# Performance work log

Measured on AMD Instinct MI355X. Metric: run time of the kernel, lower is better.

The kernel has to match this reference:

```python
import jax, jax.numpy as jnp
import numpy as np

N = 20000
E = 100000
IN_CH = 512
OUT_CH = 256
HID = 2 * OUT_CH          # 512
CAT = 5 * HID             # 2560
BN_EPS = 1e-5


def _sage(x, src, dst, w_edge, Wl, Wr, b):
    """PyG SAGEConv (mean aggr): lin_l(mean_{j->i} x_j) + lin_r(x_i).
    w_edge: per-edge float weight (0/1 mask); messages flow src -> dst."""
    msg = x[src] * w_edge[:, None]                              # [E, F]
    s = jax.ops.segment_sum(msg, dst, num_segments=N)           # [N, F]
    cnt = jax.ops.segment_sum(w_edge, dst, num_segments=N)      # [N]
    mean = s / jnp.maximum(cnt, 1.0)[:, None]
    return mean @ Wl.T + x @ Wr.T + b


def setup_inputs() -> dict:
    key = jax.random.key(0)
    ks = jax.random.split(key, 12)
    x = jax.random.normal(ks[0], (N, IN_CH), dtype=jnp.float32)
    edge_index = jax.random.randint(ks[1], (2, E), 0, N, dtype=jnp.int64)
    edge_attr = jax.random.randint(ks[2], (E,), 0, 5, dtype=jnp.int64)
    sc = 1.0 / np.sqrt(IN_CH)
    Wl5 = jax.random.uniform(ks[3], (5, HID, IN_CH), jnp.float32, -sc, sc)
    Wr5 = jax.random.uniform(ks[4], (5, HID, IN_CH), jnp.float32, -sc, sc)
    bl5 = jnp.zeros((5, HID), jnp.float32)
    sc2 = 1.0 / np.sqrt(CAT)
    Wmu_l = jax.random.uniform(ks[5], (OUT_CH, CAT), jnp.float32, -sc2, sc2)
    Wmu_r = jax.random.uniform(ks[6], (OUT_CH, CAT), jnp.float32, -sc2, sc2)
    bmu = jnp.zeros((OUT_CH,), jnp.float32)
    Wlv_l = jax.random.uniform(ks[7], (OUT_CH, CAT), jnp.float32, -sc2, sc2)
    Wlv_r = jax.random.uniform(ks[8], (OUT_CH, CAT), jnp.float32, -sc2, sc2)
    blv = jnp.zeros((OUT_CH,), jnp.float32)
    gamma = jnp.ones((CAT,), jnp.float32)
    beta = jnp.zeros((CAT,), jnp.float32)
    run_mean = jax.random.normal(ks[9], (CAT,), jnp.float32) * 0.1
    run_var = jnp.abs(jax.random.normal(ks[10], (CAT,), jnp.float32)) + 1.0
    return {"x": x, "edge_index": edge_index, "edge_attr": edge_attr,
            "Wl5": Wl5, "Wr5": Wr5, "bl5": bl5,
            "Wmu_l": Wmu_l, "Wmu_r": Wmu_r, "bmu": bmu,
            "Wlv_l": Wlv_l, "Wlv_r": Wlv_r, "blv": blv,
            "gamma": gamma, "beta": beta,
            "run_mean": run_mean, "run_var": run_var}


def reference(x, edge_index, edge_attr, Wl5, Wr5, bl5,
              Wmu_l, Wmu_r, bmu, Wlv_l, Wlv_r, blv,
              gamma, beta, run_mean, run_var):
    # eval mode: all dropouts are identity, BatchNorm uses running stats.
    src, dst = edge_index[0], edge_index[1]
    # 5 relation branches: mask edges by relation id instead of nonzero slicing
    branches = []
    for k in range(5):
        w = (edge_attr == k).astype(x.dtype)                    # [E]
        h = _sage(x, src, dst, w, Wl5[k], Wr5[k], bl5[k])       # [N, HID]
        branches.append(jax.nn.relu(h))
    h = jnp.concatenate(branches, axis=1)                       # [N, CAT]
    # BatchNorm1d (eval)
    h = (h - run_mean) * jax.lax.rsqrt(run_var + BN_EPS) * gamma + beta
    ones = jnp.ones((E,), x.dtype)
    mu = _sage(h, src, dst, ones, Wmu_l, Wmu_r, bmu)            # [N, OUT_CH]
    logvar = _sage(h, src, dst, ones, Wlv_l, Wlv_r, blv)        # [N, OUT_CH]
    return (mu, logvar)
```

## Files before the change

### kernel.cpp

```cpp
#include <hip/hip_runtime.h>
#include <stdint.h>

#define INCH 512
#define HIDW 512
#define CATW 2560
#define OUTW 256
#define BN_EPS 1e-5f
#define TS 1024

typedef __bf16 bf16x8 __attribute__((ext_vector_type(8)));
typedef float f32x4 __attribute__((ext_vector_type(4)));

__device__ __forceinline__ unsigned short f2bf(float f) {
  union { float f; unsigned u; } v; v.f = f;
  unsigned r = v.u + 0x7FFFu + ((v.u >> 16) & 1u);
  return (unsigned short)(r >> 16);
}

__device__ __forceinline__ float bf2f(unsigned short u) {
  union { unsigned u; float f; } v; v.u = ((unsigned)u) << 16; return v.f;
}

__device__ __forceinline__ void pack4(unsigned short* dst, float a, float b, float c, float d) {
  unsigned lo = (unsigned)f2bf(a) | ((unsigned)f2bf(b) << 16);
  unsigned hi = (unsigned)f2bf(c) | ((unsigned)f2bf(d) << 16);
  *reinterpret_cast<uint2*>(dst) = make_uint2(lo, hi);
}


__global__ void cvt_bf16_kernel(const float* __restrict__ in, unsigned short* __restrict__ out, int n4) {
  int g = blockIdx.x * blockDim.x + threadIdx.x;
  if (g >= n4) return;
  int base = g * 4;
  float4 v = *reinterpret_cast<const float4*>(in + base);
  pack4(out + base, v.x, v.y, v.z, v.w);
}

__global__ void pack_w1p_kernel(const float* __restrict__ Wl, const float* __restrict__ Wr,
                                unsigned short* __restrict__ out) {
  int g = blockIdx.x * blockDim.x + threadIdx.x;
  if (g >= 5 * 128 * 512) return;
  int z = g >> 16;
  int rem = g & 65535;
  int c = rem >> 9;
  int j = rem & 511;
  int kk = c * 8;
  const float* src = (kk < 512) ? (Wl + ((size_t)(z * 512 + j)) * 512 + kk)
                                : (Wr + ((size_t)(z * 512 + j)) * 512 + (kk - 512));
  float4 a = *reinterpret_cast<const float4*>(src);
  float4 b = *reinterpret_cast<const float4*>(src + 4);
  pack4(out + (size_t)g * 8, a.x, a.y, a.z, a.w);
  pack4(out + (size_t)g * 8 + 4, b.x, b.y, b.z, b.w);
}

__global__ void pack_w23p_kernel(const float* __restrict__ Wmu_l, const float* __restrict__ Wlv_l,
                                 const float* __restrict__ Wmu_r, const float* __restrict__ Wlv_r,
                                 unsigned short* __restrict__ out) {
  int g = blockIdx.x * blockDim.x + threadIdx.x;
  if (g >= 320 * 1024) return;
  int c = g >> 10;
  int j = g & 1023;
  const float* row;
  if (j < 256)       row = Wmu_l + (size_t)j * CATW;
  else if (j < 512)  row = Wlv_l + (size_t)(j - 256) * CATW;
  else if (j < 768)  row = Wmu_r + (size_t)(j - 512) * CATW;
  else               row = Wlv_r + (size_t)(j - 768) * CATW;
  const float* src = row + c * 8;
  float4 a = *reinterpret_cast<const float4*>(src);
  float4 b = *reinterpret_cast<const float4*>(src + 4);
  pack4(out + (size_t)g * 8, a.x, a.y, a.z, a.w);
  pack4(out + (size_t)g * 8 + 4, b.x, b.y, b.z, b.w);
}


__global__ void hist_kernel(const int* __restrict__ ei, const int* __restrict__ ea,
                            int* __restrict__ cnt, int E) {
  int e = blockIdx.x * 256 + threadIdx.x;
  if (e >= E) return;
  atomicAdd(&cnt[ei[E + e] * 5 + ea[e]], 1);
}

__global__ void scan1_kernel(const int* __restrict__ in, int* __restrict__ out,
                             int* __restrict__ bsum, int n) {
  __shared__ int lds[256];
  int t = threadIdx.x;
  int base = blockIdx.x * TS + t * 4;
  int4 v = make_int4(0, 0, 0, 0);
  if (base + 3 < n) v = *reinterpret_cast<const int4*>(in + base);
  else {
    if (base < n) v.x = in[base];
    if (base + 1 < n) v.y = in[base + 1];
    if (base + 2 < n) v.z = in[base + 2];
    if (base + 3 < n) v.w = in[base + 3];
  }
  int s = v.x + v.y + v.z + v.w;
  lds[t] = s;
  __syncthreads();
  for (int o = 1; o < 256; o <<= 1) {
    int a = (t >= o) ? lds[t - o] : 0;
    __syncthreads();
    lds[t] += a;
    __syncthreads();
  }
  int excl = lds[t] - s;
  if (t == 255) bsum[blockIdx.x] = lds[255];
  int e0 = excl, e1 = e0 + v.x, e2 = e1 + v.y, e3 = e2 + v.z;
  if (base < n) out[base] = e0;
  if (base + 1 < n) out[base + 1] = e1;
  if (base + 2 < n) out[base + 2] = e2;
  if (base + 3 < n) out[base + 3] = e3;
}

__global__ void scan2_kernel(int* __restrict__ bsum, int nb) {
  __shared__ int lds[128];
  int t = threadIdx.x;
  int v = (t < nb) ? bsum[t] : 0;
  lds[t] = v;
  __syncthreads();
  for (int o = 1; o < 128; o <<= 1) {
    int a = (t >= o) ? lds[t - o] : 0;
    __syncthreads();
    lds[t] += a;
    __syncthreads();
  }
  if (t < nb) bsum[t] = lds[t] - v;
}

__global__ void scan3_kernel(int* __restrict__ out, const int* __restrict__ bsum,
                             int n, int total) {
  int g = blockIdx.x * 256 + threadIdx.x;
  if (g == 0) out[n] = total;
  int base = g * 4;
  if (base >= n) return;
  int add = bsum[base / TS];
  if (base + 3 < n) {
    int4 v = *reinterpret_cast<int4*>(out + base);
    v.x += add; v.y += add; v.z += add; v.w += add;
    *reinterpret_cast<int4*>(out + base) = v;
  } else {
    for (int q = 0; q < 4 && base + q < n; ++q) out[base + q] += add;
  }
}

__global__ void fill_kernel(const int* __restrict__ ei, const int* __restrict__ ea,
                            const int* __restrict__ offs, int* __restrict__ fillc,
                            int* __restrict__ perm, int E) {
  int e = blockIdx.x * 256 + threadIdx.x;
  if (e >= E) return;
  int key = ei[E + e] * 5 + ea[e];
  int p = atomicAdd(&fillc[key], 1);
  perm[offs[key] + p] = ei[e];
}


__global__ void gather1_kernel(const unsigned short* __restrict__ xb, const int* __restrict__ offs,
                               const int* __restrict__ perm, unsigned short* __restrict__ meanb5) {
  int i = blockIdx.x;
  int k = blockIdx.y;
  int t = threadIdx.x;
  int b0 = offs[i * 5 + k], b1 = offs[i * 5 + k + 1];
  float a0 = 0.f, a1 = 0.f, a2 = 0.f, a3 = 0.f;
  for (int e = b0; e < b1; ++e) {
    int s = perm[e];
    ushort4 v = reinterpret_cast<const ushort4*>(xb + (size_t)s * 512)[t];
    a0 += bf2f(v.x); a1 += bf2f(v.y); a2 += bf2f(v.z); a3 += bf2f(v.w);
  }
  float inv = (b1 > b0) ? 1.0f / (float)(b1 - b0) : 0.0f;
  pack4(meanb5 + (size_t)i * CATW + k * 512 + t * 4, a0 * inv, a1 * inv, a2 * inv, a3 * inv);
}

__global__ void gather2_kernel(const float* __restrict__ z, const int* __restrict__ offs,
                               const int* __restrict__ perm, float* __restrict__ dout,
                               const float* __restrict__ bmu, const float* __restrict__ blv,
                               int M) {
  int i = blockIdx.x;
  int t = threadIdx.x;
  int b0 = offs[i * 5], b1 = offs[i * 5 + 5];
  float4 acc = make_float4(0.f, 0.f, 0.f, 0.f);
  for (int e = b0; e < b1; ++e) {
    int s = perm[e];
    float4 v = reinterpret_cast<const float4*>(z + (size_t)s * 512)[t];
    acc.x += v.x; acc.y += v.y; acc.z += v.z; acc.w += v.w;
  }
  float inv = (b1 > b0) ? 1.0f / (float)(b1 - b0) : 1.0f;
  int c = t * 4;
  float* op;
  const float* bp;
  if (c < 256) { op = dout + (size_t)i * OUTW + c; bp = bmu + c; }
  else         { op = dout + (size_t)M * OUTW + (size_t)i * OUTW + (c - 256); bp = blv + (c - 256); }
  float4 y = *reinterpret_cast<float4*>(op);
  float4 b = *reinterpret_cast<const float4*>(bp);
  y.x += acc.x * inv + b.x; y.y += acc.y * inv + b.y;
  y.z += acc.z * inv + b.z; y.w += acc.w * inv + b.w;
  *reinterpret_cast<float4*>(op) = y;
}

template<int MODE>
__global__ __launch_bounds__(256, 3)
void gemm_kernel(const unsigned short* __restrict__ A,
                 const unsigned short* __restrict__ A2,
                 const unsigned short* __restrict__ B,
                 unsigned short* __restrict__ hOut,
                 float* __restrict__ fOut,
                 float* __restrict__ fOut2,
                 const float* __restrict__ p0,
                 const float* __restrict__ p1,
                 const float* __restrict__ p2,
                 const float* __restrict__ p3,
                 const float* __restrict__ p4,
                 int M)
{
  constexpr int KTOT = (MODE == 0) ? (2 * INCH) : CATW;
  constexpr int KT = KTOT / 32;
  constexpr int NBLK = (MODE == 0) ? 4 : 8;
  constexpr int NC = (MODE == 0) ? 512 : 1024;

  const int nwg = gridDim.x;
  const int o = blockIdx.x;
  const int q = nwg >> 3, r = nwg & 7;
  const int xcd = o & 7;
  const int wg = (xcd < r ? xcd * (q + 1) : r * (q + 1) + (xcd - r) * q) + (o >> 3);
  const int rowBase = (wg / NBLK) * 128;
  const int nBase = (wg % NBLK) * 128;
  const int z = (MODE == 0) ? blockIdx.z : 0;
  const unsigned short* BpF = (MODE == 0) ? (B + (size_t)z * 524288) : B;

  __shared__ unsigned short As[4][4096];

  const int tid = threadIdx.x;
  const int lane = tid & 63;
  const int wv = tid >> 6;
  const int wr = wv >> 1, wc = wv & 1;
  const int lr = lane & 15, kg = lane >> 4;

  const int srow0 = (wv * 2) * 16 + (lane >> 2);
  const int srow1 = srow0 + 16;
  const int kswz = (((lane & 3) ^ ((lane >> 4) & 3)) * 8);
  int gar0 = rowBase + srow0; if (gar0 >= M) gar0 = M - 1;
  int gar1 = rowBase + srow1; if (gar1 >= M) gar1 = M - 1;

  int aslot[4];
#pragma unroll
  for (int m = 0; m < 4; ++m) {
    const int ar = wr * 64 + m * 16 + lr;
    aslot[m] = ar * 32 + ((kg ^ ((lr >> 2) & 3)) * 8);
  }

  size_t bjoff[4];
#pragma unroll
  for (int n = 0; n < 4; ++n)
    bjoff[n] = (size_t)(nBase + wc * 64 + n * 16 + lr) * 8;

  f32x4 acc[4][4] = {};

  auto stageA = [&](int slot, int kt) {
    const int kk0 = kt * 32;
    const unsigned short *a0p, *a1p;
    if (MODE == 0) {
      if (kk0 < INCH) {
        a0p = A + (size_t)gar0 * CATW + z * 512 + kk0 + kswz;
        a1p = A + (size_t)gar1 * CATW + z * 512 + kk0 + kswz;
      } else {
        a0p = A2 + (size_t)gar0 * INCH + (kk0 - INCH) + kswz;
        a1p = A2 + (size_t)gar1 * INCH + (kk0 - INCH) + kswz;
      }
    } else {
      a0p = A + (size_t)gar0 * KTOT + kk0 + kswz;
      a1p = A + (size_t)gar1 * KTOT + kk0 + kswz;
    }
    __builtin_amdgcn_global_load_lds((const void*)a0p, (void*)&As[slot][(wv * 2) * 512], 16, 0, 0);
    __builtin_amdgcn_global_load_lds((const void*)a1p, (void*)&As[slot][(wv * 2 + 1) * 512], 16, 0, 0);
  };

  auto loadB = [&](int kt, bf16x8 (&dst)[4]) {
    const size_t cbase = (size_t)((kt << 2) + kg) * NC * 8;
#pragma unroll
    for (int n = 0; n < 4; ++n)
      dst[n] = *reinterpret_cast<const bf16x8*>(BpF + cbase + bjoff[n]);
  };

  auto step = [&](int t, const bf16x8 (&bcur)[4], bf16x8 (&bnxt)[4]) {
    const int slot = t & 3;
    bf16x8 af[4];
#pragma unroll
    for (int m = 0; m < 4; ++m)
      af[m] = *reinterpret_cast<const bf16x8*>(&As[slot][aslot[m]]);
    if (t + 1 < KT) loadB(t + 1, bnxt);
    if (t + 3 < KT) stageA((t + 3) & 3, t + 3);
    __builtin_amdgcn_sched_barrier(0);
    __builtin_amdgcn_s_setprio(1);
#pragma unroll
    for (int m = 0; m < 4; ++m)
#pragma unroll
      for (int n = 0; n < 4; ++n)
        acc[m][n] = __builtin_amdgcn_mfma_f32_16x16x32_bf16(af[m], bcur[n], acc[m][n], 0, 0, 0);
    __builtin_amdgcn_s_setprio(0);
    __builtin_amdgcn_sched_barrier(0);
    __builtin_amdgcn_s_barrier();
    __builtin_amdgcn_sched_barrier(0);
  };

  bf16x8 bP[4], bQ[4];
  stageA(0, 0);
  stageA(1, 1);
  stageA(2, 2);
  __builtin_amdgcn_sched_barrier(0);
  loadB(0, bP);
  __builtin_amdgcn_sched_barrier(0);
  asm volatile("s_waitcnt vmcnt(8)" ::: "memory");
  __builtin_amdgcn_s_barrier();
  __builtin_amdgcn_sched_barrier(0);

  for (int t = 0; t < KT; t += 2) {
    step(t, bP, bQ);
    step(t + 1, bQ, bP);
  }

  if (MODE == 0) {
    unsigned short* lds16 = &As[0][0];
#pragma unroll
    for (int n = 0; n < 4; ++n) {
      const int j = wc * 64 + n * 16 + lr;
      const int ch = z * 512 + nBase + j;
      const float bias = p0[ch];
      const float scale = rsqrtf(p2[ch] + BN_EPS) * p3[ch];
      const float rm = p1[ch], be = p4[ch];
#pragma unroll
      for (int m = 0; m < 4; ++m)
#pragma unroll
        for (int rr = 0; rr < 4; ++rr) {
          const int row = wr * 64 + m * 16 + kg * 4 + rr;
          float v = acc[m][n][rr] + bias;
          v = fmaxf(v, 0.0f);
          v = (v - rm) * scale + be;
          lds16[row * 128 + (j ^ ((row & 7) << 3))] = f2bf(v);
        }
    }
    __syncthreads();
    const int trow = tid >> 4;
    const int cb = tid & 15;
#pragma unroll
    for (int p = 0; p < 8; ++p) {
      const int row = p * 16 + trow;
      const int i = rowBase + row;
      if (i < M) {
        const int scb = cb ^ (row & 7);
        uint4 v = *reinterpret_cast<const uint4*>(&lds16[row * 128 + scb * 8]);
        *reinterpret_cast<uint4*>(&hOut[(size_t)i * CATW + z * 512 + nBase + cb * 8]) = v;
      }
    }
  } else {
    float* ldsf = reinterpret_cast<float*>(&As[0][0]);
#pragma unroll
    for (int hp = 0; hp < 2; ++hp) {
      __syncthreads();
      if (wc == hp) {
#pragma unroll
        for (int n = 0; n < 4; ++n) {
          const int jl = n * 16 + lr;
#pragma unroll
          for (int m = 0; m < 4; ++m)
#pragma unroll
            for (int rr = 0; rr < 4; ++rr) {
              const int row = wr * 64 + m * 16 + kg * 4 + rr;
              ldsf[row * 64 + jl] = acc[m][n][rr];
            }
        }
      }
      __syncthreads();
      const int trow = tid >> 4, cb = tid & 15;
      const int jbase = nBase + hp * 64;
#pragma unroll
      for (int p = 0; p < 8; ++p) {
        const int row = p * 16 + trow;
        const int i = rowBase + row;
        if (i < M) {
          float4 v = *reinterpret_cast<const float4*>(&ldsf[row * 64 + cb * 4]);
          const int j = jbase + cb * 4;
          float* dst;
          if (j < 512) {
            dst = fOut + (size_t)i * 512 + j;
          } else {
            const int jj = j - 512;
            dst = (jj < OUTW) ? (fOut2 + (size_t)i * OUTW + jj)
                              : (fOut2 + (size_t)M * OUTW + (size_t)i * OUTW + (jj - OUTW));
          }
          *reinterpret_cast<float4*>(dst) = v;
        }
      }
    }
  }
}


extern "C" void kernel_launch(void* const* d_in, const int* in_sizes, int n_in,
                              void* d_out, int out_size, void* d_ws, size_t ws_size,
                              hipStream_t stream) {
  const float* x     = (const float*)d_in[0];
  const int*   ei    = (const int*)d_in[1];
  const int*   ea    = (const int*)d_in[2];
  const float* Wl5   = (const float*)d_in[3];
  const float* Wr5   = (const float*)d_in[4];
  const float* bl5   = (const float*)d_in[5];
  const float* Wmu_l = (const float*)d_in[6];
  const float* Wmu_r = (const float*)d_in[7];
  const float* bmu   = (const float*)d_in[8];
  const float* Wlv_l = (const float*)d_in[9];
  const float* Wlv_r = (const float*)d_in[10];
  const float* blv   = (const float*)d_in[11];
  const float* gamma = (const float*)d_in[12];
  const float* beta  = (const float*)d_in[13];
  const float* rmean = (const float*)d_in[14];
  const float* rvar  = (const float*)d_in[15];
  (void)n_in; (void)out_size;

  const int N = in_sizes[0] / INCH;
  const int E = in_sizes[2];
  const int NKEY = N * 5;

  char* ws = (char*)d_ws;
  size_t off = 0;
  auto take = [&](size_t bytes) { char* p = ws + off; off += (bytes + 255) & ~(size_t)255; return p; };
  unsigned short* hb = (unsigned short*)take((size_t)N * CATW * 2);
  char* U = take((size_t)N * CATW * 2);
  unsigned short* xb = (unsigned short*)take((size_t)N * 512 * 2);
  unsigned short* w1p  = (unsigned short*)take((size_t)5 * 128 * 512 * 8 * 2);
  unsigned short* w23p = (unsigned short*)take((size_t)320 * 1024 * 8 * 2);
  int* cntk  = (int*)take((size_t)NKEY * 4);
  int* offs  = (int*)take((size_t)(NKEY + 1) * 4);
  int* fillc = (int*)take((size_t)NKEY * 4);
  int* perm  = (int*)take((size_t)E * 4);
  int* bsum  = (int*)take(256 * 4);
  if (off > ws_size) return;

  unsigned short* meanb5 = (unsigned short*)U;
  float* zbuf  = (float*)U;

  cvt_bf16_kernel<<<dim3((N * INCH / 4 + 255) / 256), 256, 0, stream>>>(x, xb, N * INCH / 4);
  pack_w1p_kernel<<<dim3((5 * 128 * 512 + 255) / 256), 256, 0, stream>>>(Wl5, Wr5, w1p);
  pack_w23p_kernel<<<dim3((320 * 1024 + 255) / 256), 256, 0, stream>>>(Wmu_l, Wlv_l, Wmu_r, Wlv_r, w23p);

  hipMemsetAsync(cntk, 0, (size_t)NKEY * 4, stream);
  hipMemsetAsync(fillc, 0, (size_t)NKEY * 4, stream);
  hist_kernel<<<dim3((E + 255) / 256), 256, 0, stream>>>(ei, ea, cntk, E);
  const int nb = (NKEY + TS - 1) / TS;
  scan1_kernel<<<dim3(nb), 256, 0, stream>>>(cntk, offs, bsum, NKEY);
  scan2_kernel<<<dim3(1), 128, 0, stream>>>(bsum, nb);
  scan3_kernel<<<dim3((NKEY / 4 + 255) / 256 + 1), 256, 0, stream>>>(offs, bsum, NKEY, E);
  fill_kernel<<<dim3((E + 255) / 256), 256, 0, stream>>>(ei, ea, offs, fillc, perm, E);

  gather1_kernel<<<dim3(N, 5), 128, 0, stream>>>(xb, offs, perm, meanb5);
  const int mblk = (N + 127) / 128;
  gemm_kernel<0><<<dim3(mblk * 4, 1, 5), 256, 0, stream>>>(
      meanb5, xb, w1p, hb, nullptr, nullptr,
      bl5, rmean, rvar, gamma, beta, N);

  gemm_kernel<1><<<dim3(mblk * 8, 1, 1), 256, 0, stream>>>(
      hb, nullptr, w23p, nullptr, zbuf, (float*)d_out,
      nullptr, nullptr, nullptr, nullptr, nullptr, N);

  gather2_kernel<<<dim3(N), 128, 0, stream>>>(zbuf, offs, perm, (float*)d_out, bmu, blv, N);
}
```

Baseline: 368.9 us.

## Deepen GEMM A-staging pipeline, store intermediate z in bf16, merge gather1 branches

The GEMM main loop now uses a six-slot LDS ring with prefetch four steps ahead, and issues one barrier per two K-steps through a superstep structure. The tail steps drain outstanding loads with an explicit wait. The intermediate z buffer written by the second GEMM and read by gather2 is now bf16 rather than fp32, which halves its gather traffic at some cost in precision. gather1 loops over all five relations in one block instead of launching one block per relation. The larger LDS footprint (48KB) may lower occupancy, and the manual vmcnt accounting could be fragile.

Measured after the change: 350.7 us, median of 2. 4.9% less time.

```diff
diff --git a/kernel.cpp b/kernel.cpp
--- a/kernel.cpp
+++ b/kernel.cpp
@@ -156,31 +156,33 @@
 __global__ void gather1_kernel(const unsigned short* __restrict__ xb, const int* __restrict__ offs,
                                const int* __restrict__ perm, unsigned short* __restrict__ meanb5) {
   int i = blockIdx.x;
-  int k = blockIdx.y;
   int t = threadIdx.x;
-  int b0 = offs[i * 5 + k], b1 = offs[i * 5 + k + 1];
-  float a0 = 0.f, a1 = 0.f, a2 = 0.f, a3 = 0.f;
-  for (int e = b0; e < b1; ++e) {
-    int s = perm[e];
-    ushort4 v = reinterpret_cast<const ushort4*>(xb + (size_t)s * 512)[t];
-    a0 += bf2f(v.x); a1 += bf2f(v.y); a2 += bf2f(v.z); a3 += bf2f(v.w);
-  }
-  float inv = (b1 > b0) ? 1.0f / (float)(b1 - b0) : 0.0f;
-  pack4(meanb5 + (size_t)i * CATW + k * 512 + t * 4, a0 * inv, a1 * inv, a2 * inv, a3 * inv);
-}
-
-__global__ void gather2_kernel(const float* __restrict__ z, const int* __restrict__ offs,
+#pragma unroll
+  for (int k = 0; k < 5; ++k) {
+    int b0 = offs[i * 5 + k], b1 = offs[i * 5 + k + 1];
+    float a0 = 0.f, a1 = 0.f, a2 = 0.f, a3 = 0.f;
+    for (int e = b0; e < b1; ++e) {
+      int s = perm[e];
+      ushort4 v = reinterpret_cast<const ushort4*>(xb + (size_t)s * 512)[t];
+      a0 += bf2f(v.x); a1 += bf2f(v.y); a2 += bf2f(v.z); a3 += bf2f(v.w);
+    }
+    float inv = (b1 > b0) ? 1.0f / (float)(b1 - b0) : 0.0f;
+    pack4(meanb5 + (size_t)i * CATW + k * 512 + t * 4, a0 * inv, a1 * inv, a2 * inv, a3 * inv);
+  }
+}
+
+__global__ void gather2_kernel(const unsigned short* __restrict__ zb, const int* __restrict__ offs,
                                const int* __restrict__ perm, float* __restrict__ dout,
                                const float* __restrict__ bmu, const float* __restrict__ blv,
                                int M) {
   int i = blockIdx.x;
   int t = threadIdx.x;
   int b0 = offs[i * 5], b1 = offs[i * 5 + 5];
-  float4 acc = make_float4(0.f, 0.f, 0.f, 0.f);
+  float a0 = 0.f, a1 = 0.f, a2 = 0.f, a3 = 0.f;
   for (int e = b0; e < b1; ++e) {
     int s = perm[e];
-    float4 v = reinterpret_cast<const float4*>(z + (size_t)s * 512)[t];
-    acc.x += v.x; acc.y += v.y; acc.z += v.z; acc.w += v.w;
+    ushort4 v = reinterpret_cast<const ushort4*>(zb + (size_t)s * 512)[t];
+    a0 += bf2f(v.x); a1 += bf2f(v.y); a2 += bf2f(v.z); a3 += bf2f(v.w);
   }
   float inv = (b1 > b0) ? 1.0f / (float)(b1 - b0) : 1.0f;
   int c = t * 4;
@@ -190,8 +192,8 @@
   else         { op = dout + (size_t)M * OUTW + (size_t)i * OUTW + (c - 256); bp = blv + (c - 256); }
   float4 y = *reinterpret_cast<float4*>(op);
   float4 b = *reinterpret_cast<const float4*>(bp);
-  y.x += acc.x * inv + b.x; y.y += acc.y * inv + b.y;
-  y.z += acc.z * inv + b.z; y.w += acc.w * inv + b.w;
+  y.x += a0 * inv + b.x; y.y += a1 * inv + b.y;
+  y.z += a2 * inv + b.z; y.w += a3 * inv + b.w;
   *reinterpret_cast<float4*>(op) = y;
 }
 
@@ -201,7 +203,7 @@
                  const unsigned short* __restrict__ A2,
                  const unsigned short* __restrict__ B,
                  unsigned short* __restrict__ hOut,
-                 float* __restrict__ fOut,
+                 unsigned short* __restrict__ zbOut,
                  float* __restrict__ fOut2,
                  const float* __restrict__ p0,
                  const float* __restrict__ p1,
@@ -225,7 +227,7 @@
   const int z = (MODE == 0) ? blockIdx.z : 0;
   const unsigned short* BpF = (MODE == 0) ? (B + (size_t)z * 524288) : B;
 
-  __shared__ unsigned short As[4][4096];
+  __shared__ unsigned short As[6][4096];
 
   const int tid = threadIdx.x;
   const int lane = tid & 63;
@@ -279,42 +281,58 @@
       dst[n] = *reinterpret_cast<const bf16x8*>(BpF + cbase + bjoff[n]);
   };
 
-  auto step = [&](int t, const bf16x8 (&bcur)[4], bf16x8 (&bnxt)[4]) {
-    const int slot = t & 3;
-    bf16x8 af[4];
+  auto mfma16 = [&](const bf16x8 (&af)[4], const bf16x8 (&b)[4]) {
+    __builtin_amdgcn_s_setprio(1);
 #pragma unroll
     for (int m = 0; m < 4; ++m)
-      af[m] = *reinterpret_cast<const bf16x8*>(&As[slot][aslot[m]]);
-    if (t + 1 < KT) loadB(t + 1, bnxt);
-    if (t + 3 < KT) stageA((t + 3) & 3, t + 3);
-    __builtin_amdgcn_sched_barrier(0);
-    __builtin_amdgcn_s_setprio(1);
-#pragma unroll
-    for (int m = 0; m < 4; ++m)
 #pragma unroll
       for (int n = 0; n < 4; ++n)
-        acc[m][n] = __builtin_amdgcn_mfma_f32_16x16x32_bf16(af[m], bcur[n], acc[m][n], 0, 0, 0);
+        acc[m][n] = __builtin_amdgcn_mfma_f32_16x16x32_bf16(af[m], b[n], acc[m][n], 0, 0, 0);
     __builtin_amdgcn_s_setprio(0);
-    __builtin_amdgcn_sched_barrier(0);
+  };
+
+  auto superstep = [&](int t, bf16x8 (&bP)[4], bf16x8 (&bQ)[4], bool tail) {
+    {
+      const int slot = t % 6;
+      bf16x8 af[4];
+#pragma unroll
+      for (int m = 0; m < 4; ++m)
+        af[m] = *reinterpret_cast<const bf16x8*>(&As[slot][aslot[m]]);
+      loadB(t + 1, bQ);
+      if (t + 4 < KT) stageA((t + 4) % 6, t + 4);
+      __builtin_amdgcn_sched_barrier(0);
+      mfma16(af, bP);
+      __builtin_amdgcn_sched_barrier(0);
+    }
+    {
+      const int slot = (t + 1) % 6;
+      bf16x8 af[4];
+#pragma unroll
+      for (int m = 0; m < 4; ++m)
+        af[m] = *reinterpret_cast<const bf16x8*>(&As[slot][aslot[m]]);
+      if (t + 2 < KT) loadB(t + 2, bP);
+      if (t + 5 < KT) stageA((t + 5) % 6, t + 5);
+      __builtin_amdgcn_sched_barrier(0);
+      mfma16(af, bQ);
+      __builtin_amdgcn_sched_barrier(0);
+    }
+    if (tail) asm volatile("s_waitcnt vmcnt(0)" ::: "memory");
     __builtin_amdgcn_s_barrier();
     __builtin_amdgcn_sched_barrier(0);
   };
 
   bf16x8 bP[4], bQ[4];
-  stageA(0, 0);
-  stageA(1, 1);
-  stageA(2, 2);
+  loadB(0, bP);
+  stageA(0, 0); stageA(1, 1); stageA(2, 2); stageA(3, 3);
   __builtin_amdgcn_sched_barrier(0);
-  loadB(0, bP);
-  __builtin_amdgcn_sched_barrier(0);
-  asm volatile("s_waitcnt vmcnt(8)" ::: "memory");
+  asm volatile("s_waitcnt vmcnt(4)" ::: "memory");
   __builtin_amdgcn_s_barrier();
   __builtin_amdgcn_sched_barrier(0);
 
-  for (int t = 0; t < KT; t += 2) {
-    step(t, bP, bQ);
-    step(t + 1, bQ, bP);
-  }
+  int t = 0;
+  for (; t < KT - 4; t += 2) superstep(t, bP, bQ, false);
+  superstep(t, bP, bQ, true); t += 2;
+  superstep(t, bP, bQ, true);
 
   if (MODE == 0) {
     unsigned short* lds16 = &As[0][0];
@@ -377,15 +395,14 @@
         if (i < M) {
           float4 v = *reinterpret_cast<const float4*>(&ldsf[row * 64 + cb * 4]);
           const int j = jbase + cb * 4;
-          float* dst;
           if (j < 512) {
-            dst = fOut + (size_t)i * 512 + j;
+            pack4(zbOut + (size_t)i * 512 + j, v.x, v.y, v.z, v.w);
           } else {
             const int jj = j - 512;
-            dst = (jj < OUTW) ? (fOut2 + (size_t)i * OUTW + jj)
-                              : (fOut2 + (size_t)M * OUTW + (size_t)i * OUTW + (jj - OUTW));
+            float* dst = (jj < OUTW) ? (fOut2 + (size_t)i * OUTW + jj)
+                                     : (fOut2 + (size_t)M * OUTW + (size_t)i * OUTW + (jj - OUTW));
+            *reinterpret_cast<float4*>(dst) = v;
           }
-          *reinterpret_cast<float4*>(dst) = v;
         }
       }
     }
@@ -434,7 +451,7 @@
   if (off > ws_size) return;
 
   unsigned short* meanb5 = (unsigned short*)U;
-  float* zbuf  = (float*)U;
+  unsigned short* zb = (unsigned short*)U;
 
   cvt_bf16_kernel<<<dim3((N * INCH / 4 + 255) / 256), 256, 0, stream>>>(x, xb, N * INCH / 4);
   pack_w1p_kernel<<<dim3((5 * 128 * 512 + 255) / 256), 256, 0, stream>>>(Wl5, Wr5, w1p);
@@ -449,15 +466,15 @@
   scan3_kernel<<<dim3((NKEY / 4 + 255) / 256 + 1), 256, 0, stream>>>(offs, bsum, NKEY, E);
   fill_kernel<<<dim3((E + 255) / 256), 256, 0, stream>>>(ei, ea, offs, fillc, perm, E);
 
-  gather1_kernel<<<dim3(N, 5), 128, 0, stream>>>(xb, offs, perm, meanb5);
+  gather1_kernel<<<dim3(N), 128, 0, stream>>>(xb, offs, perm, meanb5);
   const int mblk = (N + 127) / 128;
   gemm_kernel<0><<<dim3(mblk * 4, 1, 5), 256, 0, stream>>>(
       meanb5, xb, w1p, hb, nullptr, nullptr,
       bl5, rmean, rvar, gamma, beta, N);
 
   gemm_kernel<1><<<dim3(mblk * 8, 1, 1), 256, 0, stream>>>(
-      hb, nullptr, w23p, nullptr, zbuf, (float*)d_out,
+      hb, nullptr, w23p, nullptr, zb, (float*)d_out,
       nullptr, nullptr, nullptr, nullptr, nullptr, N);
 
-  gather2_kernel<<<dim3(N), 128, 0, stream>>>(zbuf, offs, perm, (float*)d_out, bmu, blv, N);
-}
+  gather2_kernel<<<dim3(N), 128, 0, stream>>>(zb, offs, perm, (float*)d_out, bmu, blv, N);
+}
```
